# Performance work log

Hardware: AMD Instinct MI355X
Metric: run time of the kernel (lower is better)

Reference implementation:

```python
import jax, jax.numpy as jnp
import numpy as np

D_MODEL = 1024
N_HEAD = 16
HEAD_DIM = D_MODEL // N_HEAD


def setup_inputs() -> dict:
    key = jax.random.key(0)
    ks = jax.random.split(key, 12)
    B, S, D = 4, 2048, D_MODEL
    s = 1.0 / np.sqrt(D)
    inp = {
        "query": jax.random.normal(ks[0], (B, S, D), jnp.float32),
        "key": jax.random.normal(ks[1], (B, S, D), jnp.float32),
        "value": jax.random.normal(ks[2], (B, S, D), jnp.float32),
        "mask": jnp.ones((B, 1, 1, S), jnp.int32),
        "Wq": jax.random.normal(ks[3], (D, D), jnp.float32) * s,
        "bq": jnp.zeros((D,), jnp.float32),
        "Wk": jax.random.normal(ks[4], (D, D), jnp.float32) * s,
        "bk": jnp.zeros((D,), jnp.float32),
        "Wv": jax.random.normal(ks[5], (D, D), jnp.float32) * s,
        "bv": jnp.zeros((D,), jnp.float32),
        "Wo": jax.random.normal(ks[6], (D, D), jnp.float32) * s,
        "bo": jnp.zeros((D,), jnp.float32),
    }
    return inp


def _split_heads(x, W, b):
    # x: [B, S, D] -> [B, H, S, Dh]
    B, S, _ = x.shape
    out = x @ W + b
    return out.reshape(B, S, N_HEAD, HEAD_DIM).transpose(0, 2, 1, 3)


def reference(query, key, value, mask, Wq, bq, Wk, bk, Wv, bv, Wo, bo):
    B, S, D = query.shape
    q = _split_heads(query, Wq, bq)
    k = _split_heads(key, Wk, bk)
    v = _split_heads(value, Wv, bv)
    scale = 1.0 / jnp.sqrt(jnp.asarray(HEAD_DIM, q.dtype))
    scores = jnp.einsum("bhqd,bhkd->bhqk", q, k) * scale  # [B,H,S,S]
    scores = jnp.where(mask == 0, jnp.asarray(-1e9, scores.dtype), scores)
    attn = jax.nn.softmax(scores, axis=-1)  # dropout is identity in eval mode
    out = jnp.einsum("bhqk,bhkd->bhqd", attn, v)
    out = out.transpose(0, 2, 1, 3).reshape(B, S, D)
    return out @ Wo + bo
```

## Files before the change

kernel.cpp:

```cpp
#include <hip/hip_runtime.h>


typedef float  f32x4  __attribute__((ext_vector_type(4)));
typedef float  f32x16 __attribute__((ext_vector_type(16)));
typedef short  s16x8  __attribute__((ext_vector_type(8)));
typedef unsigned short u16x4 __attribute__((ext_vector_type(4)));
typedef unsigned int   u32x4 __attribute__((ext_vector_type(4)));

#define DEV static __device__ __forceinline__

DEV unsigned short f2bf(float f) {
  unsigned u = __float_as_uint(f);
  u += 0x7fffu + ((u >> 16) & 1u);
  return (unsigned short)(u >> 16);
}

DEV unsigned pk2(float lo, float hi) {
  return (unsigned)f2bf(lo) | ((unsigned)f2bf(hi) << 16);
}

DEV void gld_lds16(const void* g, void* l) {
  __builtin_amdgcn_global_load_lds(
      (const __attribute__((address_space(1))) unsigned int*)g,
      (__attribute__((address_space(3))) unsigned int*)l, 16, 0, 0);
}

__global__ __launch_bounds__(256) void wtrans_kernel(
    const float* __restrict__ W0, const float* __restrict__ W1,
    const float* __restrict__ W2, const float* __restrict__ W3,
    unsigned short* __restrict__ T0, unsigned short* __restrict__ T1,
    unsigned short* __restrict__ T2, unsigned short* __restrict__ T3)
{
  __shared__ float tile[64][65];
  const float* W; unsigned short* T;
  switch (blockIdx.z) {
    case 0: W = W0; T = T0; break;
    case 1: W = W1; T = T1; break;
    case 2: W = W2; T = T2; break;
    default: W = W3; T = T3; break;
  }
  const int bi = blockIdx.x, bj = blockIdx.y;
  const int t = threadIdx.x;
  const int c4 = (t & 15) * 4, rr = t >> 4;
  #pragma unroll
  for (int j = 0; j < 4; j++) {
    int r = j * 16 + rr;
    float4 v = *(const float4*)(W + (size_t)(bi * 64 + r) * 1024 + bj * 64 + c4);
    tile[r][c4 + 0] = v.x; tile[r][c4 + 1] = v.y;
    tile[r][c4 + 2] = v.z; tile[r][c4 + 3] = v.w;
  }
  __syncthreads();
  #pragma unroll
  for (int j = 0; j < 4; j++) {
    int n = j * 16 + rr;
    u16x4 p;
    #pragma unroll
    for (int i = 0; i < 4; i++) p[i] = f2bf(tile[c4 + i][n]);
    *(u16x4*)(T + (size_t)(bj * 64 + n) * 1024 + bi * 64 + c4) = p;
  }
}

__global__ __launch_bounds__(256) void gemm_qkv_kernel(
    const float* __restrict__ Aq, const float* __restrict__ Ak, const float* __restrict__ Av,
    const unsigned short* __restrict__ Btq, const unsigned short* __restrict__ Btk,
    const unsigned short* __restrict__ Btv,
    const float* __restrict__ pbq, const float* __restrict__ pbk, const float* __restrict__ pbv,
    unsigned short* __restrict__ Qp, unsigned short* __restrict__ Kp,
    unsigned short* __restrict__ Vtg)
{
  const int z = blockIdx.z;
  const float* A  = (z == 0) ? Aq : (z == 1) ? Ak : Av;
  const unsigned short* Bt = (z == 0) ? Btq : (z == 1) ? Btk : Btv;
  const float* bias = (z == 0) ? pbq : (z == 1) ? pbk : pbv;
  unsigned short* outp = (z == 0) ? Qp : (z == 1) ? Kp : Vtg;
  const float scale = (z == 0) ? 0.18033688011112042f : 1.0f;
  const int epi = (z == 2) ? 1 : 0;

  const int tid = threadIdx.x;
  const int lane = tid & 63, w = tid >> 6;
  const int wm = w >> 1, wn = w & 1;
  const int m0 = blockIdx.y * 128, n0 = blockIdx.x * 128;
  __shared__ __align__(16) char sA[8192];
  __shared__ __align__(16) char sB[8192];

  f32x4 acc[4][4];
  #pragma unroll
  for (int i = 0; i < 4; i++)
    #pragma unroll
    for (int j = 0; j < 4; j++)
      #pragma unroll
      for (int r = 0; r < 4; r++) acc[i][j][r] = 0.f;

  const int arow = tid >> 3;
  const int akl  = (tid & 7) * 4;
  const int brow = lane >> 2;
  const int bkl  = (lane & 3) * 8;

  for (int kt = 0; kt < 32; kt++) {
    const int k0 = kt * 32;
    #pragma unroll
    for (int j = 0; j < 4; j++) {
      int row = arow + j * 32;
      float4 v = *(const float4*)(A + (size_t)(m0 + row) * 1024 + k0 + akl);
      u16x4 p; p[0] = f2bf(v.x); p[1] = f2bf(v.y); p[2] = f2bf(v.z); p[3] = f2bf(v.w);
      *(u16x4*)(sA + row * 64 + akl * 2) = p;
    }
    #pragma unroll
    for (int j = 0; j < 2; j++) {
      int row = (w * 2 + j) * 16 + brow;
      gld_lds16(Bt + (size_t)(n0 + row) * 1024 + k0 + bkl, sB + (w * 2 + j) * 1024);
    }
    __syncthreads();
    s16x8 aF[4], bF[4];
    #pragma unroll
    for (int i = 0; i < 4; i++)
      aF[i] = *(const s16x8*)(sA + (wm * 64 + i * 16 + (lane & 15)) * 64 + (lane >> 4) * 16);
    #pragma unroll
    for (int i = 0; i < 4; i++)
      bF[i] = *(const s16x8*)(sB + (wn * 64 + i * 16 + (lane & 15)) * 64 + (lane >> 4) * 16);
    #pragma unroll
    for (int mi = 0; mi < 4; mi++)
      #pragma unroll
      for (int ni = 0; ni < 4; ni++)
        acc[mi][ni] = __builtin_amdgcn_mfma_f32_16x16x32_bf16(aF[mi], bF[ni], acc[mi][ni], 0, 0, 0);
    __syncthreads();
  }

  #pragma unroll
  for (int ni = 0; ni < 4; ni++) {
    const int gn = n0 + wn * 64 + ni * 16 + (lane & 15);
    const float bval = bias[gn];
    const int h_ = gn >> 6, d_ = gn & 63;
    #pragma unroll
    for (int mi = 0; mi < 4; mi++) {
      const int gm = m0 + wm * 64 + mi * 16 + (lane >> 4) * 4;
      const int b_ = gm >> 11, s_ = gm & 2047;
      f32x4 a = acc[mi][ni];
      if (epi == 0) {
        #pragma unroll
        for (int r = 0; r < 4; r++)
          outp[((size_t)(b_ * 16 + h_) * 2048 + (s_ + r)) * 64 + d_] =
              f2bf((a[r] + bval) * scale);
      } else {
        u16x4 p;
        #pragma unroll
        for (int r = 0; r < 4; r++) p[r] = f2bf(a[r] + bval);
        *(u16x4*)(outp + ((size_t)(b_ * 16 + h_) * 64 + d_) * 2048 + s_) = p;
      }
    }
  }
}

__global__ __launch_bounds__(256) void attn_kernel(
    const unsigned short* __restrict__ Qp, const unsigned short* __restrict__ Kp,
    const unsigned short* __restrict__ Vtg, const int* __restrict__ mask,
    unsigned short* __restrict__ ctx)
{
  constexpr int S = 2048;
  const int tid = threadIdx.x;
  const int lane = tid & 63, w = tid >> 6;
  const int hi = lane >> 5, q31 = lane & 31;
  const int bh = blockIdx.y;
  const int b = bh >> 4, h = bh & 15;
  const int q0 = blockIdx.x * 128;
  __shared__ __align__(16) char Ks[8192];
  __shared__ __align__(16) char Vts[8192];

  const int qrow = q0 + w * 32 + q31;
  const unsigned short* qptr = Qp + ((size_t)bh * S + qrow) * 64;
  s16x8 qf[4];
  #pragma unroll
  for (int ks = 0; ks < 4; ks++) qf[ks] = *(const s16x8*)(qptr + ks * 16 + hi * 8);

  f32x16 o[2];
  #pragma unroll
  for (int d = 0; d < 2; d++)
    #pragma unroll
    for (int i = 0; i < 16; i++) o[d][i] = 0.f;
  float m_run = -1e30f, l_run = 0.f;

  const int* mrow = mask + b * S;

  for (int t = 0; t < 32; t++) {
    const int kv0 = t * 64;
    #pragma unroll
    for (int j = 0; j < 2; j++) {
      const int cb = (w * 2 + j) * 1024;
      const int oo = cb + lane * 16;
      const int row = oo >> 7;
      const int c = oo & 127;
      const int srcc = (c ^ ((row & 7) << 4)) >> 1;
      gld_lds16(Kp  + ((size_t)bh * S  + kv0 + row) * 64 + srcc, Ks  + cb);
      gld_lds16(Vtg + ((size_t)bh * 64 + row) * S + kv0  + srcc, Vts + cb);
    }
    const unsigned long long mv = __ballot(mrow[kv0 + lane] != 0);
    __syncthreads();

    f32x16 sc[2];
    #pragma unroll
    for (int kvf = 0; kvf < 2; kvf++) {
      #pragma unroll
      for (int i = 0; i < 16; i++) sc[kvf][i] = 0.f;
      const int krow = kvf * 32 + q31;
      const int sw = (krow & 7) << 4;
      #pragma unroll
      for (int ks = 0; ks < 4; ks++) {
        s16x8 kf = *(const s16x8*)(Ks + krow * 128 + ((ks * 32 + hi * 16) ^ sw));
        sc[kvf] = __builtin_amdgcn_mfma_f32_32x32x16_bf16(kf, qf[ks], sc[kvf], 0, 0, 0);
      }
    }

    if (mv != ~0ull) {
      #pragma unroll
      for (int kvf = 0; kvf < 2; kvf++)
        #pragma unroll
        for (int r = 0; r < 16; r++) {
          int kvp = kvf * 32 + (r & 3) + 8 * (r >> 2) + 4 * hi;
          if (!((mv >> kvp) & 1ull)) sc[kvf][r] = -1e30f;
        }
    }

    float mloc = -1e30f;
    #pragma unroll
    for (int kvf = 0; kvf < 2; kvf++)
      #pragma unroll
      for (int r = 0; r < 16; r++) mloc = fmaxf(mloc, sc[kvf][r]);
    mloc = fmaxf(mloc, __shfl_xor(mloc, 32));
    const float mnew = fmaxf(m_run, mloc);
    const float alpha = exp2f(m_run - mnew);
    m_run = mnew;
    float psum = 0.f;
    #pragma unroll
    for (int kvf = 0; kvf < 2; kvf++)
      #pragma unroll
      for (int r = 0; r < 16; r++) {
        float p = exp2f(sc[kvf][r] - mnew);
        sc[kvf][r] = p;
        psum += p;
      }
    psum += __shfl_xor(psum, 32);
    l_run = l_run * alpha + psum;
    #pragma unroll
    for (int d = 0; d < 2; d++)
      #pragma unroll
      for (int i = 0; i < 16; i++) o[d][i] *= alpha;

    s16x8 pa[4];
    #pragma unroll
    for (int ks = 0; ks < 4; ks++) {
      const int kvf = ks >> 1;
      const int r0 = (2 * ks) & 3;
      unsigned a0 = pk2(sc[kvf][4 * r0 + 0], sc[kvf][4 * r0 + 1]);
      unsigned a1 = pk2(sc[kvf][4 * r0 + 2], sc[kvf][4 * r0 + 3]);
      unsigned b0 = pk2(sc[kvf][4 * r0 + 4], sc[kvf][4 * r0 + 5]);
      unsigned b1 = pk2(sc[kvf][4 * r0 + 6], sc[kvf][4 * r0 + 7]);
      unsigned ax0 = __shfl_xor(a0, 32), ax1 = __shfl_xor(a1, 32);
      unsigned bx0 = __shfl_xor(b0, 32), bx1 = __shfl_xor(b1, 32);
      u32x4 wv;
      wv[0] = hi ? bx0 : a0;
      wv[1] = hi ? bx1 : a1;
      wv[2] = hi ? b0  : ax0;
      wv[3] = hi ? b1  : ax1;
      union { u32x4 u; s16x8 s; } cvt; cvt.u = wv;
      pa[ks] = cvt.s;
    }

    #pragma unroll
    for (int df = 0; df < 2; df++) {
      const int vrow = df * 32 + q31;
      const int sw = (vrow & 7) << 4;
      #pragma unroll
      for (int ks = 0; ks < 4; ks++) {
        s16x8 vf = *(const s16x8*)(Vts + vrow * 128 + ((ks * 32 + hi * 16) ^ sw));
        o[df] = __builtin_amdgcn_mfma_f32_32x32x16_bf16(vf, pa[ks], o[df], 0, 0, 0);
      }
    }
    __syncthreads();
  }

  const float inv = 1.0f / l_run;
  unsigned short* cp = ctx + ((size_t)(b * S + qrow)) * 1024 + h * 64;
  #pragma unroll
  for (int df = 0; df < 2; df++)
    #pragma unroll
    for (int rq = 0; rq < 4; rq++) {
      u16x4 p;
      #pragma unroll
      for (int r2 = 0; r2 < 4; r2++) p[r2] = f2bf(o[df][rq * 4 + r2] * inv);
      *(u16x4*)(cp + df * 32 + rq * 8 + hi * 4) = p;
    }
}

__global__ __launch_bounds__(256) void gemm_out_kernel(
    const unsigned short* __restrict__ Actx, const unsigned short* __restrict__ Bt,
    const float* __restrict__ bias, float* __restrict__ outp)
{
  const int tid = threadIdx.x;
  const int lane = tid & 63, w = tid >> 6;
  const int wm = w >> 1, wn = w & 1;
  const int m0 = blockIdx.y * 128, n0 = blockIdx.x * 128;
  __shared__ __align__(16) char sA[8192];
  __shared__ __align__(16) char sB[8192];

  f32x4 acc[4][4];
  #pragma unroll
  for (int i = 0; i < 4; i++)
    #pragma unroll
    for (int j = 0; j < 4; j++)
      #pragma unroll
      for (int r = 0; r < 4; r++) acc[i][j][r] = 0.f;

  const int brow = lane >> 2;
  const int bkl  = (lane & 3) * 8;

  for (int kt = 0; kt < 32; kt++) {
    const int k0 = kt * 32;
    #pragma unroll
    for (int j = 0; j < 2; j++) {
      int row = (w * 2 + j) * 16 + brow;
      gld_lds16(Actx + (size_t)(m0 + row) * 1024 + k0 + bkl, sA + (w * 2 + j) * 1024);
      gld_lds16(Bt   + (size_t)(n0 + row) * 1024 + k0 + bkl, sB + (w * 2 + j) * 1024);
    }
    __syncthreads();
    s16x8 aF[4], bF[4];
    #pragma unroll
    for (int i = 0; i < 4; i++)
      aF[i] = *(const s16x8*)(sA + (wm * 64 + i * 16 + (lane & 15)) * 64 + (lane >> 4) * 16);
    #pragma unroll
    for (int i = 0; i < 4; i++)
      bF[i] = *(const s16x8*)(sB + (wn * 64 + i * 16 + (lane & 15)) * 64 + (lane >> 4) * 16);
    #pragma unroll
    for (int mi = 0; mi < 4; mi++)
      #pragma unroll
      for (int ni = 0; ni < 4; ni++)
        acc[mi][ni] = __builtin_amdgcn_mfma_f32_16x16x32_bf16(aF[mi], bF[ni], acc[mi][ni], 0, 0, 0);
    __syncthreads();
  }

  #pragma unroll
  for (int ni = 0; ni < 4; ni++) {
    const int gn = n0 + wn * 64 + ni * 16 + (lane & 15);
    const float bval = bias[gn];
    #pragma unroll
    for (int mi = 0; mi < 4; mi++) {
      const int gm = m0 + wm * 64 + mi * 16 + (lane >> 4) * 4;
      #pragma unroll
      for (int r = 0; r < 4; r++)
        outp[(size_t)(gm + r) * 1024 + gn] = acc[mi][ni][r] + bval;
    }
  }
}

extern "C" void kernel_launch(void* const* d_in, const int* in_sizes, int n_in,
                              void* d_out, int out_size, void* d_ws, size_t ws_size,
                              hipStream_t stream)
{
  const float* query = (const float*)d_in[0];
  const float* key_  = (const float*)d_in[1];
  const float* value = (const float*)d_in[2];
  const int*   mask  = (const int*)d_in[3];
  const float* Wq = (const float*)d_in[4];
  const float* bq = (const float*)d_in[5];
  const float* Wk = (const float*)d_in[6];
  const float* bk = (const float*)d_in[7];
  const float* Wv = (const float*)d_in[8];
  const float* bv = (const float*)d_in[9];
  const float* Wo = (const float*)d_in[10];
  const float* bo = (const float*)d_in[11];
  float* out = (float*)d_out;

  unsigned short* Wtq = (unsigned short*)d_ws;
  unsigned short* Wtk = Wtq + (1u << 20);
  unsigned short* Wtv = Wtk + (1u << 20);
  unsigned short* Wto = Wtv + (1u << 20);
  unsigned short* Qp  = Wto + (1u << 20);
  unsigned short* Kp  = Qp  + (8u << 20);
  unsigned short* Vtg = Kp  + (8u << 20);
  unsigned short* ctx = Vtg + (8u << 20);

  wtrans_kernel<<<dim3(16, 16, 4), 256, 0, stream>>>(Wq, Wk, Wv, Wo, Wtq, Wtk, Wtv, Wto);
  gemm_qkv_kernel<<<dim3(8, 64, 3), 256, 0, stream>>>(query, key_, value,
                                                      Wtq, Wtk, Wtv, bq, bk, bv,
                                                      Qp, Kp, Vtg);
  attn_kernel<<<dim3(16, 64), 256, 0, stream>>>(Qp, Kp, Vtg, mask, ctx);
  gemm_out_kernel<<<dim3(8, 64), 256, 0, stream>>>(ctx, Wto, bo, out);
}
```

Before: 485.5 us.

## Double-buffer attention K/V tiles, remap blocks for XCD locality, use hardware bf16 pack

The attention kernel now double-buffers the K/V tiles in LDS, so the global-to-LDS copy of the next tile overlaps compute on the current one. It also hoists the mask check into a single up-front full-mask test, raises wave priority around the MFMA blocks, splits the max and sum reductions into independent partial chains, and uses the native exp2 builtin. All kernels replace the software float-to-bf16 rounding with the v_cvt_pk_bf16_f32 instruction, and the GEMM and attention grids remap block IDs so neighbouring tiles land on the same XCD for cache locality. The extra buffer doubles LDS use per block, which may lower occupancy.

```diff
diff --git a/kernel.cpp b/kernel.cpp
--- a/kernel.cpp
+++ b/kernel.cpp
@@ -5,7 +5,6 @@
 typedef float  f32x16 __attribute__((ext_vector_type(16)));
 typedef short  s16x8  __attribute__((ext_vector_type(8)));
 typedef unsigned short u16x4 __attribute__((ext_vector_type(4)));
-typedef unsigned int   u32x4 __attribute__((ext_vector_type(4)));
 
 #define DEV static __device__ __forceinline__
 
@@ -15,8 +14,10 @@
   return (unsigned short)(u >> 16);
 }
 
-DEV unsigned pk2(float lo, float hi) {
-  return (unsigned)f2bf(lo) | ((unsigned)f2bf(hi) << 16);
+DEV unsigned cvtpk(float lo, float hi) {
+  unsigned r;
+  asm("v_cvt_pk_bf16_f32 %0, %1, %2" : "=v"(r) : "v"(lo), "v"(hi));
+  return r;
 }
 
 DEV void gld_lds16(const void* g, void* l) {
@@ -53,10 +54,10 @@
   #pragma unroll
   for (int j = 0; j < 4; j++) {
     int n = j * 16 + rr;
-    u16x4 p;
-    #pragma unroll
-    for (int i = 0; i < 4; i++) p[i] = f2bf(tile[c4 + i][n]);
-    *(u16x4*)(T + (size_t)(bj * 64 + n) * 1024 + bi * 64 + c4) = p;
+    uint2 p;
+    p.x = cvtpk(tile[c4 + 0][n], tile[c4 + 1][n]);
+    p.y = cvtpk(tile[c4 + 2][n], tile[c4 + 3][n]);
+    *(uint2*)(T + (size_t)(bj * 64 + n) * 1024 + bi * 64 + c4) = p;
   }
 }
 
@@ -79,7 +80,9 @@
   const int tid = threadIdx.x;
   const int lane = tid & 63, w = tid >> 6;
   const int wm = w >> 1, wn = w & 1;
-  const int m0 = blockIdx.y * 128, n0 = blockIdx.x * 128;
+  const int H = blockIdx.y * 8 + blockIdx.x;
+  const int L = (H & 7) * 64 + (H >> 3);
+  const int m0 = (L >> 3) * 128, n0 = (L & 7) * 128;
   __shared__ __align__(16) char sA[8192];
   __shared__ __align__(16) char sB[8192];
 
@@ -102,8 +105,8 @@
     for (int j = 0; j < 4; j++) {
       int row = arow + j * 32;
       float4 v = *(const float4*)(A + (size_t)(m0 + row) * 1024 + k0 + akl);
-      u16x4 p; p[0] = f2bf(v.x); p[1] = f2bf(v.y); p[2] = f2bf(v.z); p[3] = f2bf(v.w);
-      *(u16x4*)(sA + row * 64 + akl * 2) = p;
+      uint2 p; p.x = cvtpk(v.x, v.y); p.y = cvtpk(v.z, v.w);
+      *(uint2*)(sA + row * 64 + akl * 2) = p;
     }
     #pragma unroll
     for (int j = 0; j < 2; j++) {
@@ -142,10 +145,10 @@
           outp[((size_t)(b_ * 16 + h_) * 2048 + (s_ + r)) * 64 + d_] =
               f2bf((a[r] + bval) * scale);
       } else {
-        u16x4 p;
-        #pragma unroll
-        for (int r = 0; r < 4; r++) p[r] = f2bf(a[r] + bval);
-        *(u16x4*)(outp + ((size_t)(b_ * 16 + h_) * 64 + d_) * 2048 + s_) = p;
+        uint2 p;
+        p.x = cvtpk(a[0] + bval, a[1] + bval);
+        p.y = cvtpk(a[2] + bval, a[3] + bval);
+        *(uint2*)(outp + ((size_t)(b_ * 16 + h_) * 64 + d_) * 2048 + s_) = p;
       }
     }
   }
@@ -160,11 +163,13 @@
   const int tid = threadIdx.x;
   const int lane = tid & 63, w = tid >> 6;
   const int hi = lane >> 5, q31 = lane & 31;
-  const int bh = blockIdx.y;
+  const int H = blockIdx.y * 16 + blockIdx.x;
+  const int L = (H & 7) * 128 + (H >> 3);
+  const int qb = L & 15, bh = L >> 4;
   const int b = bh >> 4, h = bh & 15;
-  const int q0 = blockIdx.x * 128;
-  __shared__ __align__(16) char Ks[8192];
-  __shared__ __align__(16) char Vts[8192];
+  const int q0 = qb * 128;
+  __shared__ __align__(16) char KsB[2][8192];
+  __shared__ __align__(16) char VsB[2][8192];
 
   const int qrow = q0 + w * 32 + q31;
   const unsigned short* qptr = Qp + ((size_t)bh * S + qrow) * 64;
@@ -180,9 +185,11 @@
   float m_run = -1e30f, l_run = 0.f;
 
   const int* mrow = mask + b * S;
-
-  for (int t = 0; t < 32; t++) {
-    const int kv0 = t * 64;
+  bool all1 = true;
+  for (int t = 0; t < 32; t++) all1 &= (mrow[t * 64 + lane] != 0);
+  const bool fullmask = (__ballot(all1) == ~0ull);
+
+  auto STAGE = [&](int bsel, int kv0) {
     #pragma unroll
     for (int j = 0; j < 2; j++) {
       const int cb = (w * 2 + j) * 1024;
@@ -190,17 +197,21 @@
       const int row = oo >> 7;
       const int c = oo & 127;
       const int srcc = (c ^ ((row & 7) << 4)) >> 1;
-      gld_lds16(Kp  + ((size_t)bh * S  + kv0 + row) * 64 + srcc, Ks  + cb);
-      gld_lds16(Vtg + ((size_t)bh * 64 + row) * S + kv0  + srcc, Vts + cb);
-    }
-    const unsigned long long mv = __ballot(mrow[kv0 + lane] != 0);
-    __syncthreads();
-
+      gld_lds16(Kp  + ((size_t)bh * S  + kv0 + row) * 64 + srcc, &KsB[bsel][cb]);
+      gld_lds16(Vtg + ((size_t)bh * 64 + row) * S + kv0  + srcc, &VsB[bsel][cb]);
+    }
+  };
+
+  auto TILE = [&](const char* Ks, const char* Vts, int kv0) {
     f32x16 sc[2];
     #pragma unroll
+    for (int kvf = 0; kvf < 2; kvf++)
+      #pragma unroll
+      for (int i = 0; i < 16; i++) sc[kvf][i] = 0.f;
+
+    __builtin_amdgcn_s_setprio(1);
+    #pragma unroll
     for (int kvf = 0; kvf < 2; kvf++) {
-      #pragma unroll
-      for (int i = 0; i < 16; i++) sc[kvf][i] = 0.f;
       const int krow = kvf * 32 + q31;
       const int sw = (krow & 7) << 4;
       #pragma unroll
@@ -209,62 +220,69 @@
         sc[kvf] = __builtin_amdgcn_mfma_f32_32x32x16_bf16(kf, qf[ks], sc[kvf], 0, 0, 0);
       }
     }
-
-    if (mv != ~0ull) {
-      #pragma unroll
-      for (int kvf = 0; kvf < 2; kvf++)
+    __builtin_amdgcn_s_setprio(0);
+
+    if (!fullmask) {
+      const unsigned long long mv = __ballot(mrow[kv0 + lane] != 0);
+      if (mv != ~0ull) {
         #pragma unroll
-        for (int r = 0; r < 16; r++) {
-          int kvp = kvf * 32 + (r & 3) + 8 * (r >> 2) + 4 * hi;
-          if (!((mv >> kvp) & 1ull)) sc[kvf][r] = -1e30f;
-        }
-    }
-
-    float mloc = -1e30f;
+        for (int kvf = 0; kvf < 2; kvf++)
+          #pragma unroll
+          for (int r = 0; r < 16; r++) {
+            int kvp = kvf * 32 + (r & 3) + 8 * (r >> 2) + 4 * hi;
+            if (!((mv >> kvp) & 1ull)) sc[kvf][r] = -1e30f;
+          }
+      }
+    }
+
+    float mx[4] = {-1e30f, -1e30f, -1e30f, -1e30f};
     #pragma unroll
     for (int kvf = 0; kvf < 2; kvf++)
       #pragma unroll
-      for (int r = 0; r < 16; r++) mloc = fmaxf(mloc, sc[kvf][r]);
+      for (int r = 0; r < 16; r++) mx[r & 3] = fmaxf(mx[r & 3], sc[kvf][r]);
+    float mloc = fmaxf(fmaxf(mx[0], mx[1]), fmaxf(mx[2], mx[3]));
     mloc = fmaxf(mloc, __shfl_xor(mloc, 32));
+
     const float mnew = fmaxf(m_run, mloc);
-    const float alpha = exp2f(m_run - mnew);
+    const float alpha = __builtin_amdgcn_exp2f(m_run - mnew);
     m_run = mnew;
-    float psum = 0.f;
+    #pragma unroll
+    for (int d = 0; d < 2; d++)
+      #pragma unroll
+      for (int i = 0; i < 16; i++) o[d][i] *= alpha;
+
+    float ps[4] = {0.f, 0.f, 0.f, 0.f};
     #pragma unroll
     for (int kvf = 0; kvf < 2; kvf++)
       #pragma unroll
       for (int r = 0; r < 16; r++) {
-        float p = exp2f(sc[kvf][r] - mnew);
+        float p = __builtin_amdgcn_exp2f(sc[kvf][r] - m_run);
         sc[kvf][r] = p;
-        psum += p;
+        ps[r & 3] += p;
       }
+    float psum = (ps[0] + ps[1]) + (ps[2] + ps[3]);
     psum += __shfl_xor(psum, 32);
     l_run = l_run * alpha + psum;
-    #pragma unroll
-    for (int d = 0; d < 2; d++)
-      #pragma unroll
-      for (int i = 0; i < 16; i++) o[d][i] *= alpha;
 
     s16x8 pa[4];
     #pragma unroll
     for (int ks = 0; ks < 4; ks++) {
-      const int kvf = ks >> 1;
-      const int r0 = (2 * ks) & 3;
-      unsigned a0 = pk2(sc[kvf][4 * r0 + 0], sc[kvf][4 * r0 + 1]);
-      unsigned a1 = pk2(sc[kvf][4 * r0 + 2], sc[kvf][4 * r0 + 3]);
-      unsigned b0 = pk2(sc[kvf][4 * r0 + 4], sc[kvf][4 * r0 + 5]);
-      unsigned b1 = pk2(sc[kvf][4 * r0 + 6], sc[kvf][4 * r0 + 7]);
+      const int kvf = ks >> 1, base = (ks & 1) * 8;
+      unsigned a0 = cvtpk(sc[kvf][base + 0], sc[kvf][base + 1]);
+      unsigned a1 = cvtpk(sc[kvf][base + 2], sc[kvf][base + 3]);
+      unsigned b0 = cvtpk(sc[kvf][base + 4], sc[kvf][base + 5]);
+      unsigned b1 = cvtpk(sc[kvf][base + 6], sc[kvf][base + 7]);
       unsigned ax0 = __shfl_xor(a0, 32), ax1 = __shfl_xor(a1, 32);
       unsigned bx0 = __shfl_xor(b0, 32), bx1 = __shfl_xor(b1, 32);
-      u32x4 wv;
-      wv[0] = hi ? bx0 : a0;
-      wv[1] = hi ? bx1 : a1;
-      wv[2] = hi ? b0  : ax0;
-      wv[3] = hi ? b1  : ax1;
-      union { u32x4 u; s16x8 s; } cvt; cvt.u = wv;
-      pa[ks] = cvt.s;
-    }
-
+      union { unsigned u[4]; s16x8 s; } cv;
+      cv.u[0] = hi ? bx0 : a0;
+      cv.u[1] = hi ? bx1 : a1;
+      cv.u[2] = hi ? b0  : ax0;
+      cv.u[3] = hi ? b1  : ax1;
+      pa[ks] = cv.s;
+    }
+
+    __builtin_amdgcn_s_setprio(1);
     #pragma unroll
     for (int df = 0; df < 2; df++) {
       const int vrow = df * 32 + q31;
@@ -275,6 +293,17 @@
         o[df] = __builtin_amdgcn_mfma_f32_32x32x16_bf16(vf, pa[ks], o[df], 0, 0, 0);
       }
     }
+    __builtin_amdgcn_s_setprio(0);
+  };
+
+  STAGE(0, 0);
+  __syncthreads();
+  for (int t = 0; t < 32; t += 2) {
+    STAGE(1, (t + 1) * 64);
+    TILE(KsB[0], VsB[0], t * 64);
+    __syncthreads();
+    if (t + 2 < 32) STAGE(0, (t + 2) * 64);
+    TILE(KsB[1], VsB[1], (t + 1) * 64);
     __syncthreads();
   }
 
@@ -284,10 +313,10 @@
   for (int df = 0; df < 2; df++)
     #pragma unroll
     for (int rq = 0; rq < 4; rq++) {
-      u16x4 p;
-      #pragma unroll
-      for (int r2 = 0; r2 < 4; r2++) p[r2] = f2bf(o[df][rq * 4 + r2] * inv);
-      *(u16x4*)(cp + df * 32 + rq * 8 + hi * 4) = p;
+      uint2 pw;
+      pw.x = cvtpk(o[df][rq * 4 + 0] * inv, o[df][rq * 4 + 1] * inv);
+      pw.y = cvtpk(o[df][rq * 4 + 2] * inv, o[df][rq * 4 + 3] * inv);
+      *(uint2*)(cp + df * 32 + rq * 8 + hi * 4) = pw;
     }
 }
 
@@ -298,7 +327,9 @@
   const int tid = threadIdx.x;
   const int lane = tid & 63, w = tid >> 6;
   const int wm = w >> 1, wn = w & 1;
-  const int m0 = blockIdx.y * 128, n0 = blockIdx.x * 128;
+  const int H = blockIdx.y * 8 + blockIdx.x;
+  const int L = (H & 7) * 64 + (H >> 3);
+  const int m0 = (L >> 3) * 128, n0 = (L & 7) * 128;
   __shared__ __align__(16) char sA[8192];
   __shared__ __align__(16) char sB[8192];
 
```

New measurement: 462.7 us. -4.7%, faster.
